# Optimization experiments

Measured on AMD Instinct MI355X. Metric: run time of the kernel, lower is better.

The kernel has to match this reference:

```python
import jax, jax.numpy as jnp
import numpy as np

DN = ('NCHW', 'OIHW', 'NCHW')

def _conv(x, w, pad):
    return jax.lax.conv_general_dilated(x, w, (1, 1), [(pad, pad), (pad, pad)], dimension_numbers=DN)

def setup_inputs() -> dict:
    key = jax.random.key(0)
    ks = jax.random.split(key, 6)
    B, Cin, Csh, H, W = 4, 128, 64, 512, 512
    s = lambda fan: (2.0 / fan) ** 0.5  # kaiming-ish scale
    return {
        'feature': jax.random.normal(ks[0], (B, Cin, H, W), jnp.float32),
        'w_shared': jax.random.normal(ks[1], (Csh, Cin, 3, 3), jnp.float32) * s(Cin * 9),
        'w_cls': jax.random.normal(ks[2], (2, Csh, 1, 1), jnp.float32) * s(Csh),
        'b_cls': jnp.zeros((2,), jnp.float32),
        'w_box': jax.random.normal(ks[3], (6, Csh, 1, 1), jnp.float32) * s(Csh),
        'b_box': jnp.zeros((6,), jnp.float32),
        'w_dir': jax.random.normal(ks[4], (8, Csh, 1, 1), jnp.float32) * s(Csh),
        'b_dir': jnp.zeros((8,), jnp.float32),
        'w_scr': jax.random.normal(ks[5], (4, Csh, 1, 1), jnp.float32) * s(Csh),
        'b_scr': jnp.zeros((4,), jnp.float32),
    }

def reference(feature, w_shared, w_cls, b_cls, w_box, b_box, w_dir, b_dir, w_scr, b_scr):
    # shared 3x3 conv (no bias) + ReLU -> [B, 64, H, W]
    x = jax.nn.relu(_conv(feature, w_shared, 1))
    bias = lambda b: b[None, :, None, None]
    cls = _conv(x, w_cls, 0) + bias(b_cls)                 # [B, n_cls+1, H, W]
    box = _conv(x, w_box, 0) + bias(b_box)                 # [B, 6, H, W]
    dr = _conv(x, w_dir, 0) + bias(b_dir)                  # [B, 8, H, W]
    scr = jax.nn.sigmoid(_conv(x, w_scr, 0) + bias(b_scr)) # sigmoid_keys=['scr']
    return jnp.concatenate([cls, box, dr, scr], axis=1)    # [B, 20, H, W]
```

## Files before the change

kernel.cpp:

```cpp
#include <hip/hip_runtime.h>
#include <cstdint>
#include <cstddef>


typedef __bf16 bf16x8 __attribute__((ext_vector_type(8)));
typedef float f32x16 __attribute__((ext_vector_type(16)));
typedef float f32x4v __attribute__((ext_vector_type(4)));
typedef float f32x2v __attribute__((ext_vector_type(2)));

#define CHW (512 * 512)

__device__ __forceinline__ int swz(int s, int o) {
    int lin = (s << 5) | (o << 4);
    return lin ^ ((lin >> 1) & 0x10) ^ ((lin >> 2) & 0x60);
}

__global__ void prep_w_kernel(const float* __restrict__ w, __bf16* __restrict__ ws3) {
    int idx = blockIdx.x * 256 + threadIdx.x;
    if (idx >= 64 * 128 * 9) return;
    int tap = idx % 9;
    int cin = (idx / 9) % 128;
    int och = idx / (9 * 128);
    int hc = cin >> 4;
    int hw = (cin >> 3) & 1;
    int j  = cin & 7;
    int dst = (((hc * 9 + tap) * 2 + hw) * 64 + och) * 8 + j;
    ws3[dst] = (__bf16)w[idx];
}

#define A_OFF(p)   ((p) ? 13056 : 0)
#define AROW       2176
#define B_BASE     26112
#define WC_BASE    44544
#define BIAS_BASE  48640

__global__ __launch_bounds__(256, 3)
void det_main_kernel(const float* __restrict__ feature,
                     const __bf16* __restrict__ ws3,
                     const float* __restrict__ w_cls, const float* __restrict__ b_cls,
                     const float* __restrict__ w_box, const float* __restrict__ b_box,
                     const float* __restrict__ w_dir, const float* __restrict__ b_dir,
                     const float* __restrict__ w_scr, const float* __restrict__ b_scr,
                     float* __restrict__ out) {
    __shared__ __align__(1024) char s_all[48768];

    const int tid  = threadIdx.x;
    const int lane = tid & 63;
    const int wave = tid >> 6;
    const int l31  = lane & 31;
    const int hw   = lane >> 5;
    const int wrow2 = (wave >> 1) * 2;
    const int wcb2  = (wave & 1) * 32;

    const int bid = blockIdx.x;
    const int wg  = (bid & 7) * 512 + (bid >> 3);
    const int h_t = wg & 127;
    const int rst = wg >> 7;
    const int bz  = rst >> 3;
    const int w_t = rst & 7;
    const int h0  = h_t * 4;
    const int w0  = w_t * 64;

    const int m_o  = tid & 1;
    const int m_q  = (tid >> 1) & 15;
    const int m_rr = tid >> 5;
    const int m_r  = (m_rr < 6) ? m_rr : (m_rr - 6);
    const bool m_wr = (m_rr < 6);
    const int m_h  = h0 - 1 + m_r;
    const bool m_ok = (unsigned)m_h < 512u;
    const float* m_base = feature + (size_t)(bz * 128 + m_o * 8) * CHW
                        + (size_t)(m_ok ? m_h : 0) * 512 + (w0 + 4 * m_q);

    const int e_t   = (tid < 192) ? tid : (tid - 64);
    const bool e_wr = (tid < 192);
    const int e_sd  = e_t / 96;
    const int e_r   = (e_t % 96) >> 4;
    const int e_c   = e_t & 15;
    const int e_h   = h0 - 1 + e_r;
    const bool e_ok = ((unsigned)e_h < 512u) && (e_sd ? (w0 + 64 < 512) : (w0 > 0));
    const int e_col = e_sd ? (w0 + 64) : (w0 - 2);
    const float* e_base = feature + (size_t)(bz * 128 + e_c) * CHW
                        + (size_t)(e_ok ? e_h : 0) * 512 + (e_ok ? e_col : 0);

    f32x4v R[8];
    f32x2v E;

    auto issueA = [&](int hc) {
        const float* p = m_base + (size_t)(hc * 16) * CHW;
        #pragma unroll
        for (int j = 0; j < 8; ++j) R[j] = *(const f32x4v*)(p + (size_t)j * CHW);
        E = *(const f32x2v*)(e_base + (size_t)(hc * 16) * CHW);
    };

    auto writeA = [&](int hc) {
        char* ab = s_all + A_OFF(hc & 1);
        if (m_wr) {
            #pragma unroll
            for (int k = 0; k < 4; ++k) {
                bf16x8 g;
                #pragma unroll
                for (int j = 0; j < 8; ++j) g[j] = (__bf16)(m_ok ? R[j][k] : 0.f);
                *(bf16x8*)(ab + m_r * AROW + swz(1 + 4 * m_q + k, m_o)) = g;
            }
        }
        if (e_wr) {
            float v = e_sd ? E[0] : E[1];
            *(__bf16*)(ab + e_r * AROW + swz(e_sd ? 65 : 0, e_c >> 3) + (e_c & 7) * 2)
                = (__bf16)(e_ok ? v : 0.f);
        }
    };

    auto issueB = [&](int hc) {
        char* bb = s_all + B_BASE;
        const char* src = (const char*)ws3 + hc * 18432;
        #pragma unroll
        for (int i = 0; i < 4; ++i) {
            int g0 = i * 256 + wave * 64;
            __builtin_amdgcn_global_load_lds(
                (const __attribute__((address_space(1))) void*)(src + (size_t)(g0 + lane) * 16),
                (__attribute__((address_space(3))) void*)(bb + g0 * 16), 16, 0, 0);
        }
        if (wave < 2) {
            int g0 = 1024 + wave * 64;
            __builtin_amdgcn_global_load_lds(
                (const __attribute__((address_space(1))) void*)(src + (size_t)(g0 + lane) * 16),
                (__attribute__((address_space(3))) void*)(bb + g0 * 16), 16, 0, 0);
        }
    };

    {
        char* s_wc = s_all + WC_BASE;
        float* s_bias = (float*)(s_all + BIAS_BASE);
        int och = tid >> 3;
        int j8  = (tid & 7) * 8;
        float v[8];
        if (och < 20) {
            const float* src = (och < 2)  ? (w_cls + och * 64)
                             : (och < 8)  ? (w_box + (och - 2) * 64)
                             : (och < 16) ? (w_dir + (och - 8) * 64)
                                          : (w_scr + (och - 16) * 64);
            #pragma unroll
            for (int j = 0; j < 8; ++j) v[j] = src[j8 + j];
        } else {
            #pragma unroll
            for (int j = 0; j < 8; ++j) v[j] = 0.f;
        }
        bf16x8 wv;
        #pragma unroll
        for (int j = 0; j < 8; ++j) wv[j] = (__bf16)v[j];
        *(bf16x8*)(s_wc + och * 128 + ((j8 * 2) ^ ((och & 7) << 4))) = wv;
        if (tid < 32) {
            s_bias[tid] = (tid < 2)  ? b_cls[tid]
                        : (tid < 8)  ? b_box[tid - 2]
                        : (tid < 16) ? b_dir[tid - 8]
                        : (tid < 20) ? b_scr[tid - 16] : 0.f;
        }
    }

    f32x16 zero16;
    #pragma unroll
    for (int e = 0; e < 16; ++e) zero16[e] = 0.f;
    f32x16 acc[2][2];
    acc[0][0] = zero16; acc[0][1] = zero16; acc[1][0] = zero16; acc[1][1] = zero16;

    auto mfma_phase = [&](int hc) {
        const char* ab = s_all + A_OFF(hc & 1);
        const char* bb = s_all + B_BASE;
        #pragma unroll
        for (int tap = 0; tap < 9; ++tap) {
            const int kh = tap / 3, kw = tap % 3;
            bf16x8 Bf0 = *(const bf16x8*)(bb + (size_t)((tap * 2 + hw) * 64 +      l31) * 16);
            bf16x8 Bf1 = *(const bf16x8*)(bb + (size_t)((tap * 2 + hw) * 64 + 32 + l31) * 16);
            const int sz = swz(wcb2 + l31 + kw, hw);
            bf16x8 Af0 = *(const bf16x8*)(ab + (wrow2 + 0 + kh) * AROW + sz);
            bf16x8 Af1 = *(const bf16x8*)(ab + (wrow2 + 1 + kh) * AROW + sz);
            __builtin_amdgcn_s_setprio(1);
            acc[0][0] = __builtin_amdgcn_mfma_f32_32x32x16_bf16(Af0, Bf0, acc[0][0], 0, 0, 0);
            acc[0][1] = __builtin_amdgcn_mfma_f32_32x32x16_bf16(Af0, Bf1, acc[0][1], 0, 0, 0);
            acc[1][0] = __builtin_amdgcn_mfma_f32_32x32x16_bf16(Af1, Bf0, acc[1][0], 0, 0, 0);
            acc[1][1] = __builtin_amdgcn_mfma_f32_32x32x16_bf16(Af1, Bf1, acc[1][1], 0, 0, 0);
            __builtin_amdgcn_s_setprio(0);
        }
    };

    issueB(0);
    issueA(0);
    writeA(0);
    issueA(1);
    __builtin_amdgcn_sched_barrier(0);
    asm volatile("s_waitcnt lgkmcnt(0)" ::: "memory");
    __builtin_amdgcn_s_barrier();
    __builtin_amdgcn_sched_barrier(0);

    #pragma unroll 1
    for (int h = 0; h < 8; ++h) {
        mfma_phase(h);
        __builtin_amdgcn_sched_barrier(0);
        __builtin_amdgcn_s_barrier();
        __builtin_amdgcn_sched_barrier(0);
        if (h == 7) break;
        issueB(h + 1);
        writeA(h + 1);
        if (h < 6) issueA(h + 2);
        if (h < 6) asm volatile("s_waitcnt vmcnt(9) lgkmcnt(0)" ::: "memory");
        else       asm volatile("s_waitcnt vmcnt(0) lgkmcnt(0)" ::: "memory");
        __builtin_amdgcn_s_barrier();
        __builtin_amdgcn_sched_barrier(0);
    }

    __syncthreads();
    __bf16* X = (__bf16*)s_all;
    #pragma unroll
    for (int mt = 0; mt < 2; ++mt) {
        #pragma unroll
        for (int nt = 0; nt < 2; ++nt) {
            #pragma unroll
            for (int r = 0; r < 16; ++r) {
                float v = fmaxf(acc[mt][nt][r], 0.f);
                int mpix = (r & 3) + 8 * (r >> 2) + 4 * hw;
                int px   = (wrow2 + mt) * 64 + wcb2 + mpix;
                int chn  = nt * 32 + l31;
                *(__bf16*)((char*)X + px * 128 + ((chn * 2) ^ ((px & 7) << 4))) = (__bf16)v;
            }
        }
    }

    const char* s_wc = s_all + WC_BASE;
    const float* s_bias = (const float*)(s_all + BIAS_BASE);
    f32x16 acc2[2];
    acc2[0] = zero16; acc2[1] = zero16;
    #pragma unroll
    for (int ks = 0; ks < 4; ++ks) {
        int ch0 = ks * 16 + hw * 8;
        bf16x8 a2 = *(const bf16x8*)(s_wc + l31 * 128 + ((ch0 * 2) ^ ((l31 & 7) << 4)));
        #pragma unroll
        for (int pt = 0; pt < 2; ++pt) {
            int px = (wrow2 + pt) * 64 + wcb2 + l31;
            bf16x8 b2 = *(const bf16x8*)((const char*)X + px * 128 + ((ch0 * 2) ^ ((px & 7) << 4)));
            acc2[pt] = __builtin_amdgcn_mfma_f32_32x32x16_bf16(a2, b2, acc2[pt], 0, 0, 0);
        }
    }

    #pragma unroll
    for (int pt = 0; pt < 2; ++pt) {
        int hrow = h0 + wrow2 + pt;
        int wcol = w0 + wcb2 + l31;
        #pragma unroll
        for (int r = 0; r < 16; ++r) {
            int och = (r & 3) + 8 * (r >> 2) + 4 * hw;
            if (och < 20) {
                float v = acc2[pt][r] + s_bias[och];
                if (och >= 16) v = 1.f / (1.f + __expf(-v));
                out[(((size_t)bz * 20 + och) * 512 + hrow) * 512 + wcol] = v;
            }
        }
    }
}

extern "C" void kernel_launch(void* const* d_in, const int* in_sizes, int n_in,
                              void* d_out, int out_size, void* d_ws, size_t ws_size,
                              hipStream_t stream) {
    const float* feature  = (const float*)d_in[0];
    const float* w_shared = (const float*)d_in[1];
    const float* w_cls = (const float*)d_in[2];
    const float* b_cls = (const float*)d_in[3];
    const float* w_box = (const float*)d_in[4];
    const float* b_box = (const float*)d_in[5];
    const float* w_dir = (const float*)d_in[6];
    const float* b_dir = (const float*)d_in[7];
    const float* w_scr = (const float*)d_in[8];
    const float* b_scr = (const float*)d_in[9];
    float* out = (float*)d_out;
    __bf16* ws3 = (__bf16*)d_ws;

    prep_w_kernel<<<288, 256, 0, stream>>>(w_shared, ws3);

    det_main_kernel<<<4096, 256, 0, stream>>>(feature, ws3,
                                              w_cls, b_cls, w_box, b_box,
                                              w_dir, b_dir, w_scr, b_scr, out);
}
```

Measured before the change: 261.2 us.

## Retile conv to 2x128 pixel tiles with 512 threads and one M-tile per wave

```diff
diff --git a/kernel.cpp b/kernel.cpp
--- a/kernel.cpp
+++ b/kernel.cpp
@@ -4,9 +4,9 @@
 
 
 typedef __bf16 bf16x8 __attribute__((ext_vector_type(8)));
+typedef __bf16 bf16x4 __attribute__((ext_vector_type(4)));
 typedef float f32x16 __attribute__((ext_vector_type(16)));
 typedef float f32x4v __attribute__((ext_vector_type(4)));
-typedef float f32x2v __attribute__((ext_vector_type(2)));
 
 #define CHW (512 * 512)
 
@@ -28,13 +28,13 @@
     ws3[dst] = (__bf16)w[idx];
 }
 
-#define A_OFF(p)   ((p) ? 13056 : 0)
-#define AROW       2176
-#define B_BASE     26112
-#define WC_BASE    44544
-#define BIAS_BASE  48640
-
-__global__ __launch_bounds__(256, 3)
+#define A_OFF(p)   ((p) ? 16640 : 0)
+#define AROW       4160
+#define B_BASE     33280
+#define WC_BASE    33280
+#define BIAS_BASE  37376
+
+__global__ __launch_bounds__(512, 4)
 void det_main_kernel(const float* __restrict__ feature,
                      const __bf16* __restrict__ ws3,
                      const float* __restrict__ w_cls, const float* __restrict__ b_cls,
@@ -42,93 +42,160 @@
                      const float* __restrict__ w_dir, const float* __restrict__ b_dir,
                      const float* __restrict__ w_scr, const float* __restrict__ b_scr,
                      float* __restrict__ out) {
-    __shared__ __align__(1024) char s_all[48768];
+    __shared__ __align__(1024) char s_all[51712];
 
     const int tid  = threadIdx.x;
     const int lane = tid & 63;
     const int wave = tid >> 6;
     const int l31  = lane & 31;
     const int hw   = lane >> 5;
-    const int wrow2 = (wave >> 1) * 2;
-    const int wcb2  = (wave & 1) * 32;
+    const int wrow = wave >> 2;
+    const int wcb  = (wave & 3) * 32;
 
     const int bid = blockIdx.x;
     const int wg  = (bid & 7) * 512 + (bid >> 3);
-    const int h_t = wg & 127;
-    const int rst = wg >> 7;
-    const int bz  = rst >> 3;
-    const int w_t = rst & 7;
-    const int h0  = h_t * 4;
-    const int w0  = w_t * 64;
+    const int ck  = wg >> 9;
+    const int bz  = ck >> 1;
+    const int rem = wg & 511;
+    const int h0  = (rem >> 1) * 2;
+    const int w0  = ((ck & 1) * 2 + (rem & 1)) * 128;
 
     const int m_o  = tid & 1;
-    const int m_q  = (tid >> 1) & 15;
-    const int m_rr = tid >> 5;
-    const int m_r  = (m_rr < 6) ? m_rr : (m_rr - 6);
-    const bool m_wr = (m_rr < 6);
+    const int m_q  = (tid >> 1) & 31;
+    const int m_r  = (tid >> 6) & 3;
+    const int m_hf = tid >> 8;
     const int m_h  = h0 - 1 + m_r;
     const bool m_ok = (unsigned)m_h < 512u;
-    const float* m_base = feature + (size_t)(bz * 128 + m_o * 8) * CHW
-                        + (size_t)(m_ok ? m_h : 0) * 512 + (w0 + 4 * m_q);
-
-    const int e_t   = (tid < 192) ? tid : (tid - 64);
-    const bool e_wr = (tid < 192);
-    const int e_sd  = e_t / 96;
-    const int e_r   = (e_t % 96) >> 4;
+    const float* m_base = feature
+        + (size_t)(bz * 128 + m_o * 8 + m_hf * 4) * CHW
+        + (size_t)(m_ok ? m_h : 0) * 512 + (w0 + 4 * m_q);
+
+    const bool e_on = (tid >= 128) && (tid < 256);
+    const int e_t   = tid & 127;
+    const int e_sd  = e_t >> 6;
+    const int e_r   = (e_t >> 4) & 3;
     const int e_c   = e_t & 15;
     const int e_h   = h0 - 1 + e_r;
-    const bool e_ok = ((unsigned)e_h < 512u) && (e_sd ? (w0 + 64 < 512) : (w0 > 0));
-    const int e_col = e_sd ? (w0 + 64) : (w0 - 2);
+    const bool e_ok = e_on && ((unsigned)e_h < 512u)
+                    && (e_sd ? (w0 + 128 < 512) : (w0 > 0));
+    const int e_col = e_sd ? (w0 + 128) : (w0 - 1);
     const float* e_base = feature + (size_t)(bz * 128 + e_c) * CHW
                         + (size_t)(e_ok ? e_h : 0) * 512 + (e_ok ? e_col : 0);
 
-    f32x4v R[8];
-    f32x2v E;
+    f32x4v R[4];
+    float  E;
 
     auto issueA = [&](int hc) {
         const float* p = m_base + (size_t)(hc * 16) * CHW;
         #pragma unroll
-        for (int j = 0; j < 8; ++j) R[j] = *(const f32x4v*)(p + (size_t)j * CHW);
-        E = *(const f32x2v*)(e_base + (size_t)(hc * 16) * CHW);
+        for (int j = 0; j < 4; ++j) R[j] = *(const f32x4v*)(p + (size_t)j * CHW);
+        if (e_on) E = *(e_base + (size_t)(hc * 16) * CHW);
     };
 
     auto writeA = [&](int hc) {
         char* ab = s_all + A_OFF(hc & 1);
-        if (m_wr) {
-            #pragma unroll
-            for (int k = 0; k < 4; ++k) {
-                bf16x8 g;
-                #pragma unroll
-                for (int j = 0; j < 8; ++j) g[j] = (__bf16)(m_ok ? R[j][k] : 0.f);
-                *(bf16x8*)(ab + m_r * AROW + swz(1 + 4 * m_q + k, m_o)) = g;
-            }
-        }
-        if (e_wr) {
-            float v = e_sd ? E[0] : E[1];
-            *(__bf16*)(ab + e_r * AROW + swz(e_sd ? 65 : 0, e_c >> 3) + (e_c & 7) * 2)
-                = (__bf16)(e_ok ? v : 0.f);
+        #pragma unroll
+        for (int k = 0; k < 4; ++k) {
+            bf16x4 g;
+            #pragma unroll
+            for (int j = 0; j < 4; ++j) g[j] = (__bf16)(m_ok ? R[j][k] : 0.f);
+            *(bf16x4*)(ab + m_r * AROW + swz(1 + 4 * m_q + k, m_o) + m_hf * 8) = g;
+        }
+        if (e_on) {
+            *(__bf16*)(ab + e_r * AROW + swz(e_sd ? 129 : 0, e_c >> 3) + (e_c & 7) * 2)
+                = (__bf16)(e_ok ? E : 0.f);
         }
     };
 
     auto issueB = [&](int hc) {
         char* bb = s_all + B_BASE;
         const char* src = (const char*)ws3 + hc * 18432;
-        #pragma unroll
-        for (int i = 0; i < 4; ++i) {
-            int g0 = i * 256 + wave * 64;
-            __builtin_amdgcn_global_load_lds(
-                (const __attribute__((address_space(1))) void*)(src + (size_t)(g0 + lane) * 16),
-                (__attribute__((address_space(3))) void*)(bb + g0 * 16), 16, 0, 0);
-        }
         if (wave < 2) {
-            int g0 = 1024 + wave * 64;
-            __builtin_amdgcn_global_load_lds(
-                (const __attribute__((address_space(1))) void*)(src + (size_t)(g0 + lane) * 16),
-                (__attribute__((address_space(3))) void*)(bb + g0 * 16), 16, 0, 0);
-        }
-    };
-
-    {
+            #pragma unroll
+            for (int i = 0; i < 3; ++i) {
+                int g0 = (wave * 3 + i) * 64;
+                __builtin_amdgcn_global_load_lds(
+                    (const __attribute__((address_space(1))) void*)(src + (size_t)(g0 + lane) * 16),
+                    (__attribute__((address_space(3))) void*)(bb + g0 * 16), 16, 0, 0);
+            }
+        } else {
+            #pragma unroll
+            for (int i = 0; i < 2; ++i) {
+                int g0 = (6 + (wave - 2) * 2 + i) * 64;
+                __builtin_amdgcn_global_load_lds(
+                    (const __attribute__((address_space(1))) void*)(src + (size_t)(g0 + lane) * 16),
+                    (__attribute__((address_space(3))) void*)(bb + g0 * 16), 16, 0, 0);
+            }
+        }
+    };
+
+    f32x16 zero16;
+    #pragma unroll
+    for (int e = 0; e < 16; ++e) zero16[e] = 0.f;
+    f32x16 acc[2];
+    acc[0] = zero16; acc[1] = zero16;
+
+    auto mfma_phase = [&](int hc) {
+        const char* ab = s_all + A_OFF(hc & 1);
+        const char* bb = s_all + B_BASE;
+        #pragma unroll
+        for (int tap = 0; tap < 9; ++tap) {
+            const int kh = tap / 3, kw = tap % 3;
+            bf16x8 Bf0 = *(const bf16x8*)(bb + (size_t)((tap * 2 + hw) * 64 +      l31) * 16);
+            bf16x8 Bf1 = *(const bf16x8*)(bb + (size_t)((tap * 2 + hw) * 64 + 32 + l31) * 16);
+            bf16x8 Af  = *(const bf16x8*)(ab + (wrow + kh) * AROW + swz(wcb + l31 + kw, hw));
+            __builtin_amdgcn_s_setprio(1);
+            acc[0] = __builtin_amdgcn_mfma_f32_32x32x16_bf16(Af, Bf0, acc[0], 0, 0, 0);
+            acc[1] = __builtin_amdgcn_mfma_f32_32x32x16_bf16(Af, Bf1, acc[1], 0, 0, 0);
+            __builtin_amdgcn_s_setprio(0);
+        }
+    };
+
+    issueB(0);
+    issueA(0);
+    writeA(0);
+    issueA(1);
+    __builtin_amdgcn_sched_barrier(0);
+    asm volatile("s_waitcnt lgkmcnt(0)" ::: "memory");
+    __builtin_amdgcn_s_barrier();
+    __builtin_amdgcn_sched_barrier(0);
+
+    #pragma unroll 1
+    for (int h = 0; h < 8; ++h) {
+        mfma_phase(h);
+        __builtin_amdgcn_sched_barrier(0);
+        __builtin_amdgcn_s_barrier();
+        __builtin_amdgcn_sched_barrier(0);
+        if (h == 7) break;
+        issueB(h + 1);
+        writeA(h + 1);
+        if (h < 6) {
+            issueA(h + 2);
+            __builtin_amdgcn_sched_barrier(0);
+            if (e_on) asm volatile("s_waitcnt vmcnt(5) lgkmcnt(0)" ::: "memory");
+            else      asm volatile("s_waitcnt vmcnt(4) lgkmcnt(0)" ::: "memory");
+        } else {
+            __builtin_amdgcn_sched_barrier(0);
+            asm volatile("s_waitcnt vmcnt(0) lgkmcnt(0)" ::: "memory");
+        }
+        __builtin_amdgcn_s_barrier();
+        __builtin_amdgcn_sched_barrier(0);
+    }
+
+    __bf16* X = (__bf16*)s_all;
+    #pragma unroll
+    for (int nt = 0; nt < 2; ++nt) {
+        #pragma unroll
+        for (int r = 0; r < 16; ++r) {
+            float v = fmaxf(acc[nt][r], 0.f);
+            int mpix = (r & 3) + 8 * (r >> 2) + 4 * hw;
+            int px   = wave * 32 + mpix;
+            int chn  = nt * 32 + l31;
+            *(__bf16*)((char*)X + px * 128 + ((chn * 2) ^ ((px & 7) << 4))) = (__bf16)v;
+        }
+    }
+
+    if (tid < 256) {
         char* s_wc = s_all + WC_BASE;
         float* s_bias = (float*)(s_all + BIAS_BASE);
         int och = tid >> 3;
@@ -156,103 +223,29 @@
                         : (tid < 20) ? b_scr[tid - 16] : 0.f;
         }
     }
-
-    f32x16 zero16;
-    #pragma unroll
-    for (int e = 0; e < 16; ++e) zero16[e] = 0.f;
-    f32x16 acc[2][2];
-    acc[0][0] = zero16; acc[0][1] = zero16; acc[1][0] = zero16; acc[1][1] = zero16;
-
-    auto mfma_phase = [&](int hc) {
-        const char* ab = s_all + A_OFF(hc & 1);
-        const char* bb = s_all + B_BASE;
-        #pragma unroll
-        for (int tap = 0; tap < 9; ++tap) {
-            const int kh = tap / 3, kw = tap % 3;
-            bf16x8 Bf0 = *(const bf16x8*)(bb + (size_t)((tap * 2 + hw) * 64 +      l31) * 16);
-            bf16x8 Bf1 = *(const bf16x8*)(bb + (size_t)((tap * 2 + hw) * 64 + 32 + l31) * 16);
-            const int sz = swz(wcb2 + l31 + kw, hw);
-            bf16x8 Af0 = *(const bf16x8*)(ab + (wrow2 + 0 + kh) * AROW + sz);
-            bf16x8 Af1 = *(const bf16x8*)(ab + (wrow2 + 1 + kh) * AROW + sz);
-            __builtin_amdgcn_s_setprio(1);
-            acc[0][0] = __builtin_amdgcn_mfma_f32_32x32x16_bf16(Af0, Bf0, acc[0][0], 0, 0, 0);
-            acc[0][1] = __builtin_amdgcn_mfma_f32_32x32x16_bf16(Af0, Bf1, acc[0][1], 0, 0, 0);
-            acc[1][0] = __builtin_amdgcn_mfma_f32_32x32x16_bf16(Af1, Bf0, acc[1][0], 0, 0, 0);
-            acc[1][1] = __builtin_amdgcn_mfma_f32_32x32x16_bf16(Af1, Bf1, acc[1][1], 0, 0, 0);
-            __builtin_amdgcn_s_setprio(0);
-        }
-    };
-
-    issueB(0);
-    issueA(0);
-    writeA(0);
-    issueA(1);
-    __builtin_amdgcn_sched_barrier(0);
-    asm volatile("s_waitcnt lgkmcnt(0)" ::: "memory");
-    __builtin_amdgcn_s_barrier();
-    __builtin_amdgcn_sched_barrier(0);
-
-    #pragma unroll 1
-    for (int h = 0; h < 8; ++h) {
-        mfma_phase(h);
-        __builtin_amdgcn_sched_barrier(0);
-        __builtin_amdgcn_s_barrier();
-        __builtin_amdgcn_sched_barrier(0);
-        if (h == 7) break;
-        issueB(h + 1);
-        writeA(h + 1);
-        if (h < 6) issueA(h + 2);
-        if (h < 6) asm volatile("s_waitcnt vmcnt(9) lgkmcnt(0)" ::: "memory");
-        else       asm volatile("s_waitcnt vmcnt(0) lgkmcnt(0)" ::: "memory");
-        __builtin_amdgcn_s_barrier();
-        __builtin_amdgcn_sched_barrier(0);
-    }
-
     __syncthreads();
-    __bf16* X = (__bf16*)s_all;
-    #pragma unroll
-    for (int mt = 0; mt < 2; ++mt) {
-        #pragma unroll
-        for (int nt = 0; nt < 2; ++nt) {
-            #pragma unroll
-            for (int r = 0; r < 16; ++r) {
-                float v = fmaxf(acc[mt][nt][r], 0.f);
-                int mpix = (r & 3) + 8 * (r >> 2) + 4 * hw;
-                int px   = (wrow2 + mt) * 64 + wcb2 + mpix;
-                int chn  = nt * 32 + l31;
-                *(__bf16*)((char*)X + px * 128 + ((chn * 2) ^ ((px & 7) << 4))) = (__bf16)v;
-            }
-        }
-    }
 
     const char* s_wc = s_all + WC_BASE;
     const float* s_bias = (const float*)(s_all + BIAS_BASE);
-    f32x16 acc2[2];
-    acc2[0] = zero16; acc2[1] = zero16;
+    f32x16 acc2 = zero16;
     #pragma unroll
     for (int ks = 0; ks < 4; ++ks) {
         int ch0 = ks * 16 + hw * 8;
         bf16x8 a2 = *(const bf16x8*)(s_wc + l31 * 128 + ((ch0 * 2) ^ ((l31 & 7) << 4)));
-        #pragma unroll
-        for (int pt = 0; pt < 2; ++pt) {
-            int px = (wrow2 + pt) * 64 + wcb2 + l31;
-            bf16x8 b2 = *(const bf16x8*)((const char*)X + px * 128 + ((ch0 * 2) ^ ((px & 7) << 4)));
-            acc2[pt] = __builtin_amdgcn_mfma_f32_32x32x16_bf16(a2, b2, acc2[pt], 0, 0, 0);
-        }
-    }
-
-    #pragma unroll
-    for (int pt = 0; pt < 2; ++pt) {
-        int hrow = h0 + wrow2 + pt;
-        int wcol = w0 + wcb2 + l31;
-        #pragma unroll
-        for (int r = 0; r < 16; ++r) {
-            int och = (r & 3) + 8 * (r >> 2) + 4 * hw;
-            if (och < 20) {
-                float v = acc2[pt][r] + s_bias[och];
-                if (och >= 16) v = 1.f / (1.f + __expf(-v));
-                out[(((size_t)bz * 20 + och) * 512 + hrow) * 512 + wcol] = v;
-            }
+        int px = wave * 32 + l31;
+        bf16x8 b2 = *(const bf16x8*)((const char*)X + px * 128 + ((ch0 * 2) ^ ((px & 7) << 4)));
+        acc2 = __builtin_amdgcn_mfma_f32_32x32x16_bf16(a2, b2, acc2, 0, 0, 0);
+    }
+
+    const int hrow = h0 + wrow;
+    const int wcol = w0 + wcb + l31;
+    #pragma unroll
+    for (int r = 0; r < 16; ++r) {
+        int och = (r & 3) + 8 * (r >> 2) + 4 * hw;
+        if (och < 20) {
+            float v = acc2[r] + s_bias[och];
+            if (och >= 16) v = 1.f / (1.f + __expf(-v));
+            out[(((size_t)bz * 20 + och) * 512 + hrow) * 512 + wcol] = v;
         }
     }
 }
@@ -275,7 +268,7 @@
 
     prep_w_kernel<<<288, 256, 0, stream>>>(w_shared, ws3);
 
-    det_main_kernel<<<4096, 256, 0, stream>>>(feature, ws3,
+    det_main_kernel<<<4096, 512, 0, stream>>>(feature, ws3,
                                               w_cls, b_cls, w_box, b_box,
                                               w_dir, b_dir, w_scr, b_scr, out);
 }
```

After: 245.1 us. -6.2%, faster.
